# Kernel tuning notes

Measured on AMD Instinct MI355X. Metric: run time of the kernel, lower is better.

## Reference

```python
import jax, jax.numpy as jnp
import numpy as np

IN_F, OUT_F, R = 4096, 4096, 16
ALPHA = 32.0
SCALING = ALPHA / R


def setup_inputs() -> dict:
    key = jax.random.key(0)
    kx, kw, ka = jax.random.split(key, 3)
    x = jax.random.normal(kx, (4, 2048, IN_F), dtype=jnp.float32)
    # xavier_normal for weight: std = sqrt(2/(fan_in+fan_out))
    std = float(np.sqrt(2.0 / (IN_F + OUT_F)))
    weight = jax.random.normal(kw, (OUT_F, IN_F), dtype=jnp.float32) * std
    bias = jnp.zeros((OUT_F,), dtype=jnp.float32)
    A = jax.random.normal(ka, (R, IN_F), dtype=jnp.float32) * 0.01
    # B initialized to zeros in the module, but use small random values so the
    # LoRA path is numerically exercised for kernel correctness testing.
    B = jax.random.normal(jax.random.fold_in(key, 7), (OUT_F, R), dtype=jnp.float32) * 0.01
    return {"x": x, "weight": weight, "bias": bias, "A": A, "B": B}


def reference(x, weight, bias, A, B):
    # out = x @ W^T + bias + scaling * ((x @ A^T) @ B^T)
    out = jnp.einsum('bsi,oi->bso', x, weight) + bias
    xa = jnp.einsum('bsi,ri->bsr', x, A)           # [b, s, r] low-rank projection
    out = out + SCALING * jnp.einsum('bsr,or->bso', xa, B)
    return out
```

## Files before the change

### kernel.cpp

```cpp
#include <hip/hip_runtime.h>
#include <hip/hip_bf16.h>
#include <cstdint>
#include <cstddef>


#define IN_F   4096
#define OUT_F  4096
#define MROWS  8192
#define RLORA  16
#define LORA_SCALE 2.0f

#define CAST_BLOCKS 32768
#define FOLD_BLOCKS 4096

#define BM   256
#define BN   256
#define BKT  32
#define NT   (IN_F / BKT)

typedef __bf16 bf16x8 __attribute__((ext_vector_type(8)));
typedef float  f32x4  __attribute__((ext_vector_type(4)));
typedef int    i32x4  __attribute__((ext_vector_type(4)));

__device__ __forceinline__ unsigned short f2bf_rne(float f) {
    union { float f; unsigned u; } v; v.f = f;
    unsigned u = v.u;
    return (unsigned short)((u + 0x7FFFu + ((u >> 16) & 1u)) >> 16);
}

__device__ __forceinline__ void gl_lds16(const unsigned short* g, unsigned short* l) {
    __builtin_amdgcn_global_load_lds(
        (const __attribute__((address_space(1))) unsigned int*)g,
        (__attribute__((address_space(3))) unsigned int*)l,
        16, 0, 0);
}


__global__ void prep_kernel(const float* __restrict__ x,
                            const float* __restrict__ W,
                            const float* __restrict__ A,
                            const float* __restrict__ B,
                            unsigned short* __restrict__ xb,
                            unsigned short* __restrict__ wb) {
    __shared__ float sB[RLORA];
    const int bid = blockIdx.x;
    if (bid < CAST_BLOCKS) {
        int i = bid * blockDim.x + threadIdx.x;
        float4 v = ((const float4*)x)[i];
        ushort4 o;
        o.x = f2bf_rne(v.x); o.y = f2bf_rne(v.y);
        o.z = f2bf_rne(v.z); o.w = f2bf_rne(v.w);
        ((ushort4*)xb)[i] = o;
    } else {
        const int o = bid - CAST_BLOCKS;
        if (threadIdx.x < RLORA) sB[threadIdx.x] = B[o * RLORA + threadIdx.x];
        __syncthreads();
        const float4* W4  = (const float4*)(W + (size_t)o * IN_F);
        ushort4*      Wp4 = (ushort4*)(wb + (size_t)o * IN_F);
        for (int i4 = threadIdx.x; i4 < IN_F / 4; i4 += blockDim.x) {
            float4 w = W4[i4];
            float ax = 0.f, ay = 0.f, az = 0.f, aw = 0.f;
            #pragma unroll
            for (int r = 0; r < RLORA; ++r) {
                float4 a = ((const float4*)(A + (size_t)r * IN_F))[i4];
                float s = sB[r];
                ax += s * a.x; ay += s * a.y; az += s * a.z; aw += s * a.w;
            }
            w.x += LORA_SCALE * ax; w.y += LORA_SCALE * ay;
            w.z += LORA_SCALE * az; w.w += LORA_SCALE * aw;
            ushort4 ov;
            ov.x = f2bf_rne(w.x); ov.y = f2bf_rne(w.y);
            ov.z = f2bf_rne(w.z); ov.w = f2bf_rne(w.w);
            Wp4[i4] = ov;
        }
    }
}


__global__ __launch_bounds__(512, 2)
void gemm_bt_bias(const unsigned short* __restrict__ Xb,
                  const unsigned short* __restrict__ Wb,
                  const float* __restrict__ bias,
                  float* __restrict__ out) {
    __shared__ __align__(16) unsigned short smem[4 * 16384];

    const int tid  = threadIdx.x;
    const int wave = tid >> 6;
    const int lane = tid & 63;
    const int quad = lane >> 4;
    const int r16  = lane & 15;
    const int wm   = wave >> 2;
    const int wn   = wave & 3;

    const int bid = blockIdx.x;
    const int xcd = bid & 7;
    const int t   = bid >> 3;
    const int n0  = (xcd * 2 + (t & 1)) * BN;
    const int m0  = (t >> 1) * BM;

    const int q0  = wave * 128 + lane;
    const int q1  = q0 + 64;
    const int r0  = q0 >> 2, k0c = (q0 & 3) ^ ((r0 >> 1) & 3);
    const int r1  = q1 >> 2, k1c = (q1 & 3) ^ ((r1 >> 1) & 3);

    const unsigned short* gA0 = Xb + (size_t)(m0 + r0) * IN_F + k0c * 8;
    const unsigned short* gA1 = Xb + (size_t)(m0 + r1) * IN_F + k1c * 8;
    const unsigned short* gB0 = Wb + (size_t)(n0 + r0) * IN_F + k0c * 8;
    const unsigned short* gB1 = Wb + (size_t)(n0 + r1) * IN_F + k1c * 8;

    unsigned short* const lA0 = smem + wave * 1024;
    unsigned short* const lA1 = lA0 + 512;
    unsigned short* const lB0 = smem + 8192 + wave * 1024;
    unsigned short* const lB1 = lB0 + 512;

    const unsigned slot  = (unsigned)(quad ^ ((r16 >> 1) & 3));
    const unsigned aoff  = (unsigned)((wm * 128 + r16) * 64) + slot * 16;
    const unsigned boff  = 16384u + (unsigned)((wn * 64 + r16) * 64) + slot * 16;
    const unsigned sbase = (unsigned)(size_t)
        ((__attribute__((address_space(3))) unsigned short*)smem);

    f32x4 acc[8][4] = {};
    i32x4 aE[8], bE[4], aO[8], bO[4];

#define STAGE(TILE) {                                                    \
    const unsigned off = (unsigned)(((TILE) & 3) << 14);                 \
    gl_lds16(gA0, lA0 + off); gl_lds16(gA1, lA1 + off);                  \
    gl_lds16(gB0, lB0 + off); gl_lds16(gB1, lB1 + off);                  \
    gA0 += BKT; gA1 += BKT; gB0 += BKT; gB1 += BKT; }

#define RD_LO(AV, BV, S) {                                               \
    const unsigned bufb_ = sbase + ((unsigned)((S) & 3) << 15);          \
    const unsigned ab_ = bufb_ + aoff, bb_ = bufb_ + boff;               \
    asm volatile("ds_read_b128 %0, %1"             : "=v"(BV[0]) : "v"(bb_)); \
    asm volatile("ds_read_b128 %0, %1 offset:1024" : "=v"(BV[1]) : "v"(bb_)); \
    asm volatile("ds_read_b128 %0, %1 offset:2048" : "=v"(BV[2]) : "v"(bb_)); \
    asm volatile("ds_read_b128 %0, %1 offset:3072" : "=v"(BV[3]) : "v"(bb_)); \
    asm volatile("ds_read_b128 %0, %1"             : "=v"(AV[0]) : "v"(ab_)); \
    asm volatile("ds_read_b128 %0, %1 offset:1024" : "=v"(AV[1]) : "v"(ab_)); \
    asm volatile("ds_read_b128 %0, %1 offset:2048" : "=v"(AV[2]) : "v"(ab_)); \
    asm volatile("ds_read_b128 %0, %1 offset:3072" : "=v"(AV[3]) : "v"(ab_)); }

#define RD_HI(AV, S) {                                                   \
    const unsigned bufb_ = sbase + ((unsigned)((S) & 3) << 15);          \
    const unsigned ab_ = bufb_ + aoff;                                   \
    asm volatile("ds_read_b128 %0, %1 offset:4096" : "=v"(AV[4]) : "v"(ab_)); \
    asm volatile("ds_read_b128 %0, %1 offset:5120" : "=v"(AV[5]) : "v"(ab_)); \
    asm volatile("ds_read_b128 %0, %1 offset:6144" : "=v"(AV[6]) : "v"(ab_)); \
    asm volatile("ds_read_b128 %0, %1 offset:7168" : "=v"(AV[7]) : "v"(ab_)); }

#define CLUSTER(AV, BV, MLO, MHI) {                                      \
    _Pragma("unroll")                                                    \
    for (int mi = MLO; mi < MHI; ++mi) {                                 \
        const bf16x8 a_ = __builtin_bit_cast(bf16x8, AV[mi]);            \
        _Pragma("unroll")                                                \
        for (int nj = 0; nj < 4; ++nj)                                   \
            acc[mi][nj] = __builtin_amdgcn_mfma_f32_16x16x32_bf16(       \
                a_, __builtin_bit_cast(bf16x8, BV[nj]), acc[mi][nj], 0, 0, 0); \
    } }

    STAGE(0) STAGE(1) STAGE(2)
    asm volatile("s_waitcnt vmcnt(4)" ::: "memory");
    __builtin_amdgcn_s_barrier();
    RD_LO(aE, bE, 0)
    asm volatile("s_waitcnt lgkmcnt(0)" ::: "memory");
    __builtin_amdgcn_sched_barrier(0);

    for (int p = 0; p < NT - 2; p += 2) {
        RD_HI(aE, p)
        RD_LO(aO, bO, p + 1)
        STAGE(p + 3)
        __builtin_amdgcn_sched_barrier(0);
        __builtin_amdgcn_s_setprio(1);
        CLUSTER(aE, bE, 0, 4)
        asm volatile("s_waitcnt lgkmcnt(8)" ::: "memory");
        __builtin_amdgcn_sched_barrier(0);
        CLUSTER(aE, bE, 4, 8)
        __builtin_amdgcn_s_setprio(0);
        __builtin_amdgcn_sched_barrier(0);
        asm volatile("s_waitcnt lgkmcnt(0)" ::: "memory");
        __builtin_amdgcn_sched_barrier(0);
        asm volatile("s_waitcnt vmcnt(4)" ::: "memory");
        __builtin_amdgcn_s_barrier();

        RD_HI(aO, p + 1)
        RD_LO(aE, bE, p + 2)
        if (p + 4 < NT) STAGE(p + 4)
        __builtin_amdgcn_sched_barrier(0);
        __builtin_amdgcn_s_setprio(1);
        CLUSTER(aO, bO, 0, 4)
        asm volatile("s_waitcnt lgkmcnt(8)" ::: "memory");
        __builtin_amdgcn_sched_barrier(0);
        CLUSTER(aO, bO, 4, 8)
        __builtin_amdgcn_s_setprio(0);
        __builtin_amdgcn_sched_barrier(0);
        asm volatile("s_waitcnt lgkmcnt(0)" ::: "memory");
        __builtin_amdgcn_sched_barrier(0);
        if (p + 4 < NT) { asm volatile("s_waitcnt vmcnt(4)" ::: "memory"); }
        else            { asm volatile("s_waitcnt vmcnt(0)" ::: "memory"); }
        __builtin_amdgcn_s_barrier();
    }

    RD_HI(aE, NT - 2)
    RD_LO(aO, bO, NT - 1)
    __builtin_amdgcn_sched_barrier(0);
    __builtin_amdgcn_s_setprio(1);
    CLUSTER(aE, bE, 0, 4)
    asm volatile("s_waitcnt lgkmcnt(8)" ::: "memory");
    __builtin_amdgcn_sched_barrier(0);
    CLUSTER(aE, bE, 4, 8)
    __builtin_amdgcn_s_setprio(0);
    __builtin_amdgcn_sched_barrier(0);
    asm volatile("s_waitcnt lgkmcnt(0)" ::: "memory");
    __builtin_amdgcn_sched_barrier(0);
    asm volatile("s_waitcnt vmcnt(0)" ::: "memory");
    __builtin_amdgcn_s_barrier();

    RD_HI(aO, NT - 1)
    __builtin_amdgcn_sched_barrier(0);
    __builtin_amdgcn_s_setprio(1);
    CLUSTER(aO, bO, 0, 4)
    asm volatile("s_waitcnt lgkmcnt(0)" ::: "memory");
    __builtin_amdgcn_sched_barrier(0);
    CLUSTER(aO, bO, 4, 8)
    __builtin_amdgcn_s_setprio(0);

#undef STAGE
#undef RD_LO
#undef RD_HI
#undef CLUSTER

    float bv[4];
    #pragma unroll
    for (int nj = 0; nj < 4; ++nj)
        bv[nj] = bias[n0 + wn * 64 + nj * 16 + r16];

    #pragma unroll
    for (int mi = 0; mi < 8; ++mi) {
        #pragma unroll
        for (int i = 0; i < 4; ++i) {
            const int mg = m0 + wm * 128 + mi * 16 + quad * 4 + i;
            float* orow = out + (size_t)mg * OUT_F + (n0 + wn * 64 + r16);
            #pragma unroll
            for (int nj = 0; nj < 4; ++nj)
                orow[nj * 16] = acc[mi][nj][i] + bv[nj];
        }
    }
}


extern "C" void kernel_launch(void* const* d_in, const int* in_sizes, int n_in,
                              void* d_out, int out_size, void* d_ws, size_t ws_size,
                              hipStream_t stream) {
    const float* x    = (const float*)d_in[0];
    const float* W    = (const float*)d_in[1];
    const float* bias = (const float*)d_in[2];
    const float* A    = (const float*)d_in[3];
    const float* B    = (const float*)d_in[4];
    float* out = (float*)d_out;

    unsigned short* xb = (unsigned short*)d_ws;
    unsigned short* wb = xb + (size_t)MROWS * IN_F;

    prep_kernel<<<CAST_BLOCKS + FOLD_BLOCKS, 256, 0, stream>>>(x, W, A, B, xb, wb);
    gemm_bt_bias<<<(MROWS / BM) * (OUT_F / BN), 512, 0, stream>>>(xb, wb, bias, out);
}
```

Baseline: 531.2 us.

## Move LoRA path into GEMM: compute xA in-kernel, add via rank-16 MFMA epilogue

The LoRA update is no longer folded into W during prep. The prep kernel becomes a plain grid-stride cast of x and W to bf16. The GEMM kernel now computes x·A^T for its own row block with MFMAs before the main loop, keeps it in LDS, and adds scale·B through a rank-16 MFMA step before the bias epilogue. This removes the per-element 16-term fold over W in prep. In exchange, every block re-reads its x rows over the full K dimension, duplicating the projection across the 16 N-tiles that share each row block. It also quantizes xA and B to bf16, which changes rounding.

After: 713.9 us. 1.34x slower.

```diff
diff --git a/kernel.cpp b/kernel.cpp
--- a/kernel.cpp
+++ b/kernel.cpp
@@ -10,9 +10,6 @@
 #define RLORA  16
 #define LORA_SCALE 2.0f
 
-#define CAST_BLOCKS 32768
-#define FOLD_BLOCKS 4096
-
 #define BM   256
 #define BN   256
 #define BKT  32
@@ -35,54 +32,44 @@
         16, 0, 0);
 }
 
-
-__global__ void prep_kernel(const float* __restrict__ x,
-                            const float* __restrict__ W,
-                            const float* __restrict__ A,
-                            const float* __restrict__ B,
-                            unsigned short* __restrict__ xb,
-                            unsigned short* __restrict__ wb) {
-    __shared__ float sB[RLORA];
-    const int bid = blockIdx.x;
-    if (bid < CAST_BLOCKS) {
-        int i = bid * blockDim.x + threadIdx.x;
-        float4 v = ((const float4*)x)[i];
+__device__ __forceinline__ int cvtpk(float lo, float hi) {
+    int r;
+    asm volatile("v_cvt_pk_bf16_f32 %0, %1, %2" : "=v"(r) : "v"(lo), "v"(hi));
+    return r;
+}
+
+
+#define XF4   8388608u
+#define TOTF4 12582912u
+#define CAST_GRID 2048
+
+__global__ void cast_xw(const float* __restrict__ x,
+                        const float* __restrict__ W,
+                        unsigned short* __restrict__ xb,
+                        unsigned short* __restrict__ wbc) {
+    const unsigned stride = CAST_GRID * 256;
+    for (unsigned i = blockIdx.x * 256 + threadIdx.x; i < TOTF4; i += stride) {
+        float4 v;
+        if (i < XF4) v = ((const float4*)x)[i];
+        else         v = ((const float4*)W)[i - XF4];
         ushort4 o;
         o.x = f2bf_rne(v.x); o.y = f2bf_rne(v.y);
         o.z = f2bf_rne(v.z); o.w = f2bf_rne(v.w);
-        ((ushort4*)xb)[i] = o;
-    } else {
-        const int o = bid - CAST_BLOCKS;
-        if (threadIdx.x < RLORA) sB[threadIdx.x] = B[o * RLORA + threadIdx.x];
-        __syncthreads();
-        const float4* W4  = (const float4*)(W + (size_t)o * IN_F);
-        ushort4*      Wp4 = (ushort4*)(wb + (size_t)o * IN_F);
-        for (int i4 = threadIdx.x; i4 < IN_F / 4; i4 += blockDim.x) {
-            float4 w = W4[i4];
-            float ax = 0.f, ay = 0.f, az = 0.f, aw = 0.f;
-            #pragma unroll
-            for (int r = 0; r < RLORA; ++r) {
-                float4 a = ((const float4*)(A + (size_t)r * IN_F))[i4];
-                float s = sB[r];
-                ax += s * a.x; ay += s * a.y; az += s * a.z; aw += s * a.w;
-            }
-            w.x += LORA_SCALE * ax; w.y += LORA_SCALE * ay;
-            w.z += LORA_SCALE * az; w.w += LORA_SCALE * aw;
-            ushort4 ov;
-            ov.x = f2bf_rne(w.x); ov.y = f2bf_rne(w.y);
-            ov.z = f2bf_rne(w.z); ov.w = f2bf_rne(w.w);
-            Wp4[i4] = ov;
-        }
+        if (i < XF4) ((ushort4*)xb)[i] = o;
+        else         ((ushort4*)wbc)[i - XF4] = o;
     }
 }
 
 
 __global__ __launch_bounds__(512, 2)
 void gemm_bt_bias(const unsigned short* __restrict__ Xb,
-                  const unsigned short* __restrict__ Wb,
+                  const unsigned short* __restrict__ Wbc,
                   const float* __restrict__ bias,
+                  const float* __restrict__ Asrc,
+                  const float* __restrict__ Bsrc,
                   float* __restrict__ out) {
-    __shared__ __align__(16) unsigned short smem[4 * 16384];
+    __shared__ __align__(16) unsigned short smem[4 * 16384 + 4096];
+    unsigned short* const xa_sh = smem + 4 * 16384;
 
     const int tid  = threadIdx.x;
     const int wave = tid >> 6;
@@ -98,15 +85,44 @@
     const int n0  = (xcd * 2 + (t & 1)) * BN;
     const int m0  = (t >> 1) * BM;
 
+    {
+        const int R0 = m0 + wm * 128 + wn * 32;
+        const unsigned short* xp = Xb + (size_t)(R0 + r16) * IN_F + quad * 8;
+        const float*          ap = Asrc + (size_t)r16 * IN_F + quad * 8;
+        f32x4 xa0 = {}, xa1 = {};
+        #pragma unroll 4
+        for (int s = 0; s < NT; ++s) {
+            const i32x4 xv0 = *(const i32x4*)xp;
+            const i32x4 xv1 = *(const i32x4*)(xp + 16 * IN_F);
+            const f32x4 a0  = *(const f32x4*)ap;
+            const f32x4 a1  = *(const f32x4*)(ap + 4);
+            xp += BKT; ap += BKT;
+            i32x4 abw;
+            abw[0] = cvtpk(a0[0], a0[1]); abw[1] = cvtpk(a0[2], a0[3]);
+            abw[2] = cvtpk(a1[0], a1[1]); abw[3] = cvtpk(a1[2], a1[3]);
+            xa0 = __builtin_amdgcn_mfma_f32_16x16x32_bf16(
+                __builtin_bit_cast(bf16x8, xv0), __builtin_bit_cast(bf16x8, abw), xa0, 0, 0, 0);
+            xa1 = __builtin_amdgcn_mfma_f32_16x16x32_bf16(
+                __builtin_bit_cast(bf16x8, xv1), __builtin_bit_cast(bf16x8, abw), xa1, 0, 0, 0);
+        }
+        const int rb = wm * 128 + wn * 32;
+        #pragma unroll
+        for (int i = 0; i < 4; ++i) {
+            xa_sh[(rb +      quad * 4 + i) * 16 + r16] = f2bf_rne(xa0[i]);
+            xa_sh[(rb + 16 + quad * 4 + i) * 16 + r16] = f2bf_rne(xa1[i]);
+        }
+        __syncthreads();
+    }
+
     const int q0  = wave * 128 + lane;
     const int q1  = q0 + 64;
     const int r0  = q0 >> 2, k0c = (q0 & 3) ^ ((r0 >> 1) & 3);
     const int r1  = q1 >> 2, k1c = (q1 & 3) ^ ((r1 >> 1) & 3);
 
-    const unsigned short* gA0 = Xb + (size_t)(m0 + r0) * IN_F + k0c * 8;
-    const unsigned short* gA1 = Xb + (size_t)(m0 + r1) * IN_F + k1c * 8;
-    const unsigned short* gB0 = Wb + (size_t)(n0 + r0) * IN_F + k0c * 8;
-    const unsigned short* gB1 = Wb + (size_t)(n0 + r1) * IN_F + k1c * 8;
+    const unsigned short* gA0 = Xb  + (size_t)(m0 + r0) * IN_F + k0c * 8;
+    const unsigned short* gA1 = Xb  + (size_t)(m0 + r1) * IN_F + k1c * 8;
+    const unsigned short* gB0 = Wbc + (size_t)(n0 + r0) * IN_F + k0c * 8;
+    const unsigned short* gB1 = Wbc + (size_t)(n0 + r1) * IN_F + k1c * 8;
 
     unsigned short* const lA0 = smem + wave * 1024;
     unsigned short* const lA1 = lA0 + 512;
@@ -229,6 +245,40 @@
 #undef RD_HI
 #undef CLUSTER
 
+    {
+        i32x4 aL[8], bL[4];
+        #pragma unroll
+        for (int mi = 0; mi < 8; ++mi) {
+            i32x4 v = {};
+            if (quad < 2)
+                v = *(const i32x4*)(xa_sh + (wm * 128 + mi * 16 + r16) * 16 + quad * 8);
+            aL[mi] = v;
+        }
+        #pragma unroll
+        for (int nj = 0; nj < 4; ++nj) {
+            f32x4 b0 = {}, b1 = {};
+            if (quad < 2) {
+                const float* bp = Bsrc + (size_t)(n0 + wn * 64 + nj * 16 + r16) * RLORA + quad * 8;
+                b0 = *(const f32x4*)bp;
+                b1 = *(const f32x4*)(bp + 4);
+            }
+            i32x4 w;
+            w[0] = cvtpk(LORA_SCALE * b0[0], LORA_SCALE * b0[1]);
+            w[1] = cvtpk(LORA_SCALE * b0[2], LORA_SCALE * b0[3]);
+            w[2] = cvtpk(LORA_SCALE * b1[0], LORA_SCALE * b1[1]);
+            w[3] = cvtpk(LORA_SCALE * b1[2], LORA_SCALE * b1[3]);
+            bL[nj] = w;
+        }
+        #pragma unroll
+        for (int mi = 0; mi < 8; ++mi) {
+            const bf16x8 a_ = __builtin_bit_cast(bf16x8, aL[mi]);
+            #pragma unroll
+            for (int nj = 0; nj < 4; ++nj)
+                acc[mi][nj] = __builtin_amdgcn_mfma_f32_16x16x32_bf16(
+                    a_, __builtin_bit_cast(bf16x8, bL[nj]), acc[mi][nj], 0, 0, 0);
+        }
+    }
+
     float bv[4];
     #pragma unroll
     for (int nj = 0; nj < 4; ++nj)
@@ -258,9 +308,10 @@
     const float* B    = (const float*)d_in[4];
     float* out = (float*)d_out;
 
-    unsigned short* xb = (unsigned short*)d_ws;
-    unsigned short* wb = xb + (size_t)MROWS * IN_F;
-
-    prep_kernel<<<CAST_BLOCKS + FOLD_BLOCKS, 256, 0, stream>>>(x, W, A, B, xb, wb);
-    gemm_bt_bias<<<(MROWS / BM) * (OUT_F / BN), 512, 0, stream>>>(xb, wb, bias, out);
-}
+    unsigned short* xb  = (unsigned short*)d_ws;
+    unsigned short* wbc = xb + (size_t)MROWS * IN_F;
+
+    cast_xw<<<CAST_GRID, 256, 0, stream>>>(x, W, xb, wbc);
+    gemm_bt_bias<<<(MROWS / BM) * (OUT_F / BN), 512, 0, stream>>>(
+        xb, wbc, bias, A, B, out);
+}
```
